# Kernel optimization log

Measured on AMD Instinct MI355X. Metric: run time of the kernel, lower is better.

The kernel has to match this reference:

```python
import jax, jax.numpy as jnp
import numpy as np

HID, LAT, B, T, E, NB, V = 256, 128, 32, 32, 2048, 10, 6
M = T * E + 1  # message buffer rows; row 0 = zero padding


def _linear_params(key, fan_in, fan_out):
    k1, k2 = jax.random.split(key)
    w = jax.random.normal(k1, (fan_out, fan_in), jnp.float32) * 0.05
    b = jax.random.normal(k2, (fan_out,), jnp.float32) * 0.05
    return w, b


def setup_inputs() -> dict:
    key = jax.random.key(0)
    ks = jax.random.split(key, 20)
    inp = {}
    inp["tree_latent_vec"] = jax.random.normal(ks[0], (B, LAT), jnp.float32)
    inp["nei_idx_h"] = jax.random.randint(ks[1], (T, E, NB), 0, M, jnp.int32)
    inp["nei_idx_o"] = jax.random.randint(ks[2], (T, E, NB), 0, M, jnp.int32)
    inp["cur_labels"] = jax.random.randint(ks[3], (T, E), 0, V, jnp.int32)
    inp["contexts"] = jax.random.randint(ks[4], (T, E), 0, B, jnp.int32)
    inp["direction"] = jax.random.randint(ks[5], (T, E), 0, 2, jnp.int32)
    inp["pred_targets_step"] = jax.random.randint(ks[6], (T, E), 0, V, jnp.int32)
    inp["root_labels"] = jax.random.randint(ks[7], (B,), 0, V, jnp.int32)
    inp["root_nei_idx"] = jax.random.randint(ks[8], (B, NB), 0, M, jnp.int32)
    inp["Wz_w"], inp["Wz_b"] = _linear_params(ks[9], HID + V, HID)
    inp["Wr_w"], inp["Wr_b"] = _linear_params(ks[10], V, HID)
    inp["Ur_w"], inp["Ur_b"] = _linear_params(ks[11], HID, HID)
    inp["Wh_w"], inp["Wh_b"] = _linear_params(ks[12], HID + V, HID)
    inp["W_w"], inp["W_b"] = _linear_params(ks[13], HID + LAT, HID)
    inp["Wo_w"], inp["Wo_b"] = _linear_params(ks[14], HID, V)
    inp["U_w"], inp["U_b"] = _linear_params(ks[15], HID + LAT, HID)
    inp["Uo_w"], inp["Uo_b"] = _linear_params(ks[16], HID, 1)
    inp["Ui_w"], inp["Ui_b"] = _linear_params(ks[17], HID + V, HID)
    return inp


def reference(tree_latent_vec, Wz_w, Wz_b, Wr_w, Wr_b, Ur_w, Ur_b, Wh_w, Wh_b,
              W_w, W_b, Wo_w, Wo_b, U_w, U_b, Uo_w, Uo_b, Ui_w, Ui_b,
              nei_idx_h, nei_idx_o, cur_labels, contexts, direction,
              pred_targets_step, root_labels, root_nei_idx):
    cur_x_all = jax.nn.one_hot(cur_labels, V, dtype=jnp.float32)  # [T,E,V]

    def gru(x, h_nei):  # JTNN tree-GRU: x [E,V], h_nei [E,NB,HID]
        sum_h = h_nei.sum(axis=1)
        z = jax.nn.sigmoid(jnp.concatenate([x, sum_h], -1) @ Wz_w.T + Wz_b)
        r = jax.nn.sigmoid((x @ Wr_w.T + Wr_b)[:, None, :]
                           + h_nei @ Ur_w.T + Ur_b)
        gated = (r * h_nei).sum(axis=1)
        pre_h = jnp.tanh(jnp.concatenate([x, gated], -1) @ Wh_w.T + Wh_b)
        return (1.0 - z) * sum_h + z * pre_h

    def step(H, xs):
        t, nih, nio, x = xs
        h_nei = H[nih]                   # [E,NB,HID] gather
        new_h = gru(x, h_nei)            # [E,HID]
        cur_o = H[nio].sum(axis=1)       # [E,HID]
        write_idx = 1 + t * E + jnp.arange(E, dtype=jnp.int32)
        H = H.at[write_idx].set(new_h)   # scatter new messages
        return H, (new_h, cur_o)

    H0 = jnp.zeros((M, HID), jnp.float32)
    ts = jnp.arange(T, dtype=jnp.int32)
    H_final, (new_h_all, cur_o_all) = jax.lax.scan(
        step, H0, (ts, nei_idx_h, nei_idx_o, cur_x_all))

    # ---- word (pred) head ----
    pred_hid = jnp.concatenate(
        [jnp.zeros((B, HID), jnp.float32), new_h_all.reshape(-1, HID)], 0)
    pred_ctx = jnp.concatenate(
        [jnp.arange(B, dtype=jnp.int32), contexts.reshape(-1)], 0)
    pred_tgt = jnp.concatenate([root_labels, pred_targets_step.reshape(-1)], 0)
    pred_mask = jnp.concatenate(
        [jnp.ones((B,), jnp.float32),
         (direction.reshape(-1) == 1).astype(jnp.float32)], 0)
    inp = jnp.concatenate([pred_hid, tree_latent_vec[pred_ctx]], -1)
    pred_scores = jax.nn.relu(inp @ W_w.T + W_b) @ Wo_w.T + Wo_b  # [N,V]
    logp = jax.nn.log_softmax(pred_scores, axis=-1)
    ce = -jnp.take_along_axis(logp, pred_tgt[:, None], axis=1)[:, 0]
    pred_loss = jnp.sum(ce * pred_mask) / B
    preds = jnp.argmax(pred_scores, axis=1)
    pred_acc = jnp.sum((preds == pred_tgt).astype(jnp.float32) * pred_mask) \
        / jnp.sum(pred_mask)

    # ---- stop head ----
    root_x = jax.nn.one_hot(root_labels, V, dtype=jnp.float32)
    root_o = H_final[root_nei_idx].sum(axis=1)                    # [B,HID]
    stop_hid = jnp.concatenate(
        [jnp.concatenate([cur_x_all, cur_o_all], -1).reshape(-1, V + HID),
         jnp.concatenate([root_x, root_o], -1)], 0)
    stop_ctx = jnp.concatenate(
        [contexts.reshape(-1), jnp.arange(B, dtype=jnp.int32)], 0)
    stop_tgt = jnp.concatenate(
        [direction.reshape(-1).astype(jnp.float32),
         jnp.zeros((B,), jnp.float32)], 0)
    h1 = jax.nn.relu(stop_hid @ Ui_w.T + Ui_b)
    inp2 = jnp.concatenate([h1, tree_latent_vec[stop_ctx]], -1)
    s = (jax.nn.relu(inp2 @ U_w.T + U_b) @ Uo_w.T + Uo_b)[:, 0]
    # BCEWithLogits, reduction='sum'
    stop_loss = jnp.sum(jnp.maximum(s, 0.0) - s * stop_tgt
                        + jnp.log1p(jnp.exp(-jnp.abs(s)))) / B
    stops = (s >= 0).astype(jnp.float32)
    stop_acc = jnp.mean((stops == stop_tgt).astype(jnp.float32))

    return jnp.stack([pred_loss, stop_loss,
                      jax.lax.stop_gradient(pred_acc),
                      jax.lax.stop_gradient(stop_acc)])
```

## Files before the change

kernel.cpp:

```cpp
#include <hip/hip_runtime.h>
#include <math.h>

#define HID 256
#define LAT 128
#define BB  32
#define TT  32
#define EE  2048
#define NBR 10
#define VV  6
#define TE  (TT*EE)
#define NROWS (TE + BB)
#define MROWS (TE + 1)

typedef __attribute__((ext_vector_type(8))) short bfrag;
typedef __attribute__((ext_vector_type(4))) float ffrag;

__device__ __forceinline__ float sigmoidf_(float x) { return 1.0f / (1.0f + expf(-x)); }

__device__ __forceinline__ float bf2f(unsigned short u) {
    union { unsigned int i; float f; } x; x.i = ((unsigned int)u) << 16; return x.f;
}
__device__ __forceinline__ unsigned short f2bf(float f) {
    union { float f; unsigned int i; } x; x.f = f;
    unsigned int r = x.i + 0x7FFFu + ((x.i >> 16) & 1u);
    return (unsigned short)(r >> 16);
}

__global__ __launch_bounds__(256) void prep_all(
    const float* __restrict__ Wz, const float* __restrict__ Wh,
    const float* __restrict__ Ur, const float* __restrict__ Ui,
    const float* __restrict__ Ww, const float* __restrict__ Uw,
    unsigned short* __restrict__ dWz, unsigned short* __restrict__ dWh,
    unsigned short* __restrict__ dUr, unsigned short* __restrict__ dUi,
    unsigned short* __restrict__ dWw, unsigned short* __restrict__ dUw)
{
    const int n = blockIdx.x, k = threadIdx.x;
    const float* s; unsigned short* d; int ldw, koff;
    switch (blockIdx.y) {
        case 0:  s = Wz; d = dWz; ldw = 262; koff = VV; break;
        case 1:  s = Wh; d = dWh; ldw = 262; koff = VV; break;
        case 2:  s = Ur; d = dUr; ldw = 256; koff = 0;  break;
        case 3:  s = Ui; d = dUi; ldw = 262; koff = VV; break;
        case 4:  s = Ww; d = dWw; ldw = 384; koff = 0;  break;
        default: s = Uw; d = dUw; ldw = 384; koff = 0;  break;
    }
    d[n * 256 + k] = f2bf(s[(size_t)n * ldw + koff + k]);
}

__global__ __launch_bounds__(256) void prep_cols(
    const float* __restrict__ Wz_w, const float* __restrict__ Wz_b,
    const float* __restrict__ Wh_w, const float* __restrict__ Wh_b,
    const float* __restrict__ Wr_w, const float* __restrict__ Wr_b,
    const float* __restrict__ Ur_b,
    const float* __restrict__ Ui_w, const float* __restrict__ Ui_b,
    float* __restrict__ zcol, float* __restrict__ hcol,
    float* __restrict__ rcol, float* __restrict__ icol)
{
    const int v = blockIdx.x, h = threadIdx.x;
    zcol[v * 256 + h] = Wz_w[h * 262 + v] + Wz_b[h];
    hcol[v * 256 + h] = Wh_w[h * 262 + v] + Wh_b[h];
    rcol[v * 256 + h] = Wr_w[h * VV + v] + Wr_b[h] + Ur_b[h];
    icol[v * 256 + h] = Ui_w[h * 262 + v] + Ui_b[h];
}

__global__ __launch_bounds__(256) void lat_gemm2(
    const float* __restrict__ lat,
    const float* __restrict__ W0, const float* __restrict__ W1,
    float* __restrict__ out0, float* __restrict__ out1)
{
    const int b = blockIdx.x, h = threadIdx.x;
    const float* W = blockIdx.y ? W1 : W0;
    float* out     = blockIdx.y ? out1 : out0;
    float acc = 0.f;
    #pragma unroll 4
    for (int k = 0; k < LAT; ++k)
        acc += lat[b * LAT + k] * W[h * 384 + 256 + k];
    out[b * 256 + h] = acc;
}

#define SFP 268
#define SHP 280

__global__ __launch_bounds__(512) void step_fused(
    const unsigned short* __restrict__ Hb,
    const unsigned short* __restrict__ Ub,
    const int* __restrict__ nih, const int* __restrict__ nio,
    const int* __restrict__ labels,
    const float* __restrict__ rcol, const float* __restrict__ zcol,
    const float* __restrict__ hcol,
    const unsigned short* __restrict__ Wzb,
    const unsigned short* __restrict__ Whb,
    const unsigned short* __restrict__ Urb,
    unsigned short* __restrict__ HbW, unsigned short* __restrict__ UbW,
    unsigned short* __restrict__ curOb,
    int rowg_base)
{
    __shared__ float          s_sum[16][SFP];
    __shared__ unsigned short s_gat[16][SHP];
    __shared__ unsigned short s_nh [16][SHP];
    __shared__ int s_idxh[16][NBR];
    __shared__ int s_idxo[16][NBR];
    __shared__ int s_lbl[16];

    const int tid = threadIdx.x;
    const int e0  = blockIdx.x * 16;

    if (tid < 160) {
        s_idxh[tid / NBR][tid % NBR] = nih[e0 * NBR + tid];
        s_idxo[tid / NBR][tid % NBR] = nio[e0 * NBR + tid];
    }
    if (tid >= 160 && tid < 176) s_lbl[tid - 160] = labels[e0 + tid - 160];
    __syncthreads();

    const int w = tid >> 6;
    const int l = tid & 63;

    {
        const int el = w * 2 + (l >> 5);
        const int h0 = (l & 31) * 8;
        float s[8], g[8], o[8], rc[8];
        #pragma unroll
        for (int j = 0; j < 8; ++j) { s[j] = 0.f; g[j] = 0.f; o[j] = 0.f; }
        const int lb = s_lbl[el];
        #pragma unroll
        for (int j = 0; j < 8; ++j) rc[j] = rcol[lb * 256 + h0 + j];

        #pragma unroll
        for (int nb = 0; nb < NBR; ++nb) {
            const int ih = s_idxh[el][nb];
            if ((unsigned)(ih - rowg_base) >= (unsigned)EE) {
                uint4 hv = *reinterpret_cast<const uint4*>(Hb + (size_t)ih * 256 + h0);
                uint4 uv = *reinterpret_cast<const uint4*>(Ub + (size_t)ih * 256 + h0);
                const unsigned short* hp = reinterpret_cast<const unsigned short*>(&hv);
                const unsigned short* up = reinterpret_cast<const unsigned short*>(&uv);
                #pragma unroll
                for (int j = 0; j < 8; ++j) {
                    const float hf = bf2f(hp[j]);
                    s[j] += hf;
                    g[j] += hf * sigmoidf_(rc[j] + bf2f(up[j]));
                }
            }
            const int io = s_idxo[el][nb];
            if ((unsigned)(io - rowg_base) >= (unsigned)EE) {
                uint4 ov = *reinterpret_cast<const uint4*>(Hb + (size_t)io * 256 + h0);
                const unsigned short* op = reinterpret_cast<const unsigned short*>(&ov);
                #pragma unroll
                for (int j = 0; j < 8; ++j) o[j] += bf2f(op[j]);
            }
        }
        *reinterpret_cast<float4*>(&s_sum[el][h0])     = make_float4(s[0], s[1], s[2], s[3]);
        *reinterpret_cast<float4*>(&s_sum[el][h0 + 4]) = make_float4(s[4], s[5], s[6], s[7]);
        union { unsigned short u[8]; uint4 v; } gu, ou;
        #pragma unroll
        for (int j = 0; j < 8; ++j) { gu.u[j] = f2bf(g[j]); ou.u[j] = f2bf(o[j]); }
        *reinterpret_cast<uint4*>(&s_gat[el][h0]) = gu.v;
        *reinterpret_cast<uint4*>(curOb + (size_t)(e0 + el) * 256 + h0) = ou.v;
    }
    __syncthreads();

    const int ar  = l & 15;
    const int kg  = (l >> 4) * 8;
    const int nb0 = w * 32;

    ffrag zacc[2], pacc[2];
    #pragma unroll
    for (int nt = 0; nt < 2; ++nt) {
        zacc[nt] = (ffrag){0.f, 0.f, 0.f, 0.f};
        pacc[nt] = (ffrag){0.f, 0.f, 0.f, 0.f};
    }
    #pragma unroll
    for (int ks = 0; ks < 8; ++ks) {
        const int k0 = ks * 32 + kg;
        bfrag az;
        const float* ap = &s_sum[ar][k0];
        #pragma unroll
        for (int j = 0; j < 8; ++j) az[j] = (short)f2bf(ap[j]);
        bfrag ah = *reinterpret_cast<const bfrag*>(&s_gat[ar][k0]);
        #pragma unroll
        for (int nt = 0; nt < 2; ++nt) {
            const int n = nb0 + nt * 16 + ar;
            bfrag bz = *reinterpret_cast<const bfrag*>(Wzb + (size_t)n * 256 + k0);
            bfrag bh = *reinterpret_cast<const bfrag*>(Whb + (size_t)n * 256 + k0);
            zacc[nt] = __builtin_amdgcn_mfma_f32_16x16x32_bf16(az, bz, zacc[nt], 0, 0, 0);
            pacc[nt] = __builtin_amdgcn_mfma_f32_16x16x32_bf16(ah, bh, pacc[nt], 0, 0, 0);
        }
    }

    #pragma unroll
    for (int nt = 0; nt < 2; ++nt) {
        const int n = nb0 + nt * 16 + (l & 15);
        #pragma unroll
        for (int r = 0; r < 4; ++r) {
            const int m  = (l >> 4) * 4 + r;
            const int lb = s_lbl[m];
            const float z  = sigmoidf_(zacc[nt][r] + zcol[lb * 256 + n]);
            const float ph = tanhf(pacc[nt][r] + hcol[lb * 256 + n]);
            const float nh = (1.f - z) * s_sum[m][n] + z * ph;
            s_nh[m][n] = f2bf(nh);
        }
    }
    __syncthreads();

    {
        const int row = tid >> 5, c8 = (tid & 31) * 8;
        uint4 v = *reinterpret_cast<const uint4*>(&s_nh[row][c8]);
        *reinterpret_cast<uint4*>(HbW + (size_t)(rowg_base + e0 + row) * 256 + c8) = v;
    }

    ffrag uacc[2];
    #pragma unroll
    for (int nt = 0; nt < 2; ++nt) uacc[nt] = (ffrag){0.f, 0.f, 0.f, 0.f};
    #pragma unroll
    for (int ks = 0; ks < 8; ++ks) {
        const int k0 = ks * 32 + kg;
        bfrag a = *reinterpret_cast<const bfrag*>(&s_nh[ar][k0]);
        #pragma unroll
        for (int nt = 0; nt < 2; ++nt) {
            const int n = nb0 + nt * 16 + ar;
            bfrag b = *reinterpret_cast<const bfrag*>(Urb + (size_t)n * 256 + k0);
            uacc[nt] = __builtin_amdgcn_mfma_f32_16x16x32_bf16(a, b, uacc[nt], 0, 0, 0);
        }
    }
    #pragma unroll
    for (int nt = 0; nt < 2; ++nt) {
        const int n = nb0 + nt * 16 + (l & 15);
        #pragma unroll
        for (int r = 0; r < 4; ++r) {
            const int m = (l >> 4) * 4 + r;
            s_gat[m][n] = f2bf(uacc[nt][r]);
        }
    }
    __syncthreads();
    {
        const int row = tid >> 5, c8 = (tid & 31) * 8;
        uint4 v = *reinterpret_cast<const uint4*>(&s_gat[row][c8]);
        *reinterpret_cast<uint4*>(UbW + (size_t)(rowg_base + e0 + row) * 256 + c8) = v;
    }
}

template<int EPI>
__global__ __launch_bounds__(256) void hgemm(
    const unsigned short* __restrict__ A, int M,
    const unsigned short* __restrict__ Wb,
    const int* __restrict__ lab1, const int* __restrict__ lab2,
    const float* __restrict__ icol,
    unsigned short* __restrict__ C)
{
    __shared__ unsigned short sbuf[64 * 264];
    __shared__ int s_lb[64];

    const int tid = threadIdx.x;
    const int m0  = blockIdx.x * 64;

    if (EPI == 1 && tid < 64) {
        const int r = m0 + tid;
        int lb = 0;
        if (r < M) lb = (r < TE) ? lab1[r] : lab2[r - TE];
        s_lb[tid] = lb;
    }

    const int w  = tid >> 6;
    const int l  = tid & 63;
    const int ar = l & 15;
    const int kg = (l >> 4) * 8;
    const int lrow = tid >> 2;
    const int lcol = (tid & 3) * 8;

    ffrag acc[4][4];
    #pragma unroll
    for (int mt = 0; mt < 4; ++mt)
        #pragma unroll
        for (int nt = 0; nt < 4; ++nt)
            acc[mt][nt] = (ffrag){0.f, 0.f, 0.f, 0.f};

    for (int kc = 0; kc < 8; ++kc) {
        const int k0 = kc * 32;
        uint4 av = make_uint4(0u, 0u, 0u, 0u);
        if (m0 + lrow < M)
            av = *reinterpret_cast<const uint4*>(A + (size_t)(m0 + lrow) * 256 + k0 + lcol);
        if (kc) __syncthreads();
        *reinterpret_cast<uint4*>(&sbuf[lrow * 40 + lcol]) = av;
        __syncthreads();
        bfrag a[4];
        #pragma unroll
        for (int mt = 0; mt < 4; ++mt)
            a[mt] = *reinterpret_cast<const bfrag*>(&sbuf[(mt * 16 + ar) * 40 + kg]);
        #pragma unroll
        for (int nt = 0; nt < 4; ++nt) {
            const int n = w * 64 + nt * 16 + ar;
            bfrag b = *reinterpret_cast<const bfrag*>(Wb + (size_t)n * 256 + k0 + kg);
            #pragma unroll
            for (int mt = 0; mt < 4; ++mt)
                acc[mt][nt] = __builtin_amdgcn_mfma_f32_16x16x32_bf16(a[mt], b, acc[mt][nt], 0, 0, 0);
        }
    }
    __syncthreads();

    #pragma unroll
    for (int mt = 0; mt < 4; ++mt) {
        #pragma unroll
        for (int nt = 0; nt < 4; ++nt) {
            const int n = w * 64 + nt * 16 + (l & 15);
            #pragma unroll
            for (int r = 0; r < 4; ++r) {
                const int m = mt * 16 + (l >> 4) * 4 + r;
                float v = acc[mt][nt][r];
                if (EPI == 1) v = fmaxf(v + icol[s_lb[m] * 256 + n], 0.f);
                sbuf[m * 264 + n] = f2bf(v);
            }
        }
    }
    __syncthreads();
    {
        const int row = tid >> 2;
        const int cb  = (tid & 3) * 64;
        if (m0 + row < M) {
            #pragma unroll
            for (int q = 0; q < 8; ++q) {
                const int col = cb + q * 8;
                uint4 v = *reinterpret_cast<const uint4*>(&sbuf[row * 264 + col]);
                *reinterpret_cast<uint4*>(C + (size_t)(m0 + row) * 256 + col) = v;
            }
        }
    }
}

__global__ __launch_bounds__(256) void root_o_kernel(
    const unsigned short* __restrict__ Hb, const int* __restrict__ rni,
    unsigned short* __restrict__ dst)
{
    const int b = blockIdx.x, h = threadIdx.x;
    float o = 0.f;
    #pragma unroll
    for (int nb = 0; nb < NBR; ++nb)
        o += bf2f(Hb[(size_t)rni[b * NBR + nb] * 256 + h]);
    dst[(size_t)b * 256 + h] = f2bf(o);
}

__global__ __launch_bounds__(256) void pred_head(
    const unsigned short* __restrict__ pre, const float* __restrict__ latW,
    const float* __restrict__ W_b,
    const float* __restrict__ Wo_w, const float* __restrict__ Wo_b,
    const int* __restrict__ contexts, const int* __restrict__ direction,
    const int* __restrict__ ptgt, const int* __restrict__ root_labels,
    float* __restrict__ part)
{
    const int r = blockIdx.x;
    const int h = threadIdx.x;
    int tgt;
    float mask, v;
    if (r < TE) {
        const int c = contexts[r];
        tgt = ptgt[r];
        mask = (direction[r] == 1) ? 1.f : 0.f;
        v = bf2f(pre[(size_t)r * 256 + h]) + latW[c * 256 + h] + W_b[h];
    } else {
        const int i = r - TE;
        tgt = root_labels[i];
        mask = 1.f;
        v = latW[i * 256 + h] + W_b[h];
    }
    v = fmaxf(v, 0.f);

    __shared__ float red[VV][4];
    const int lane = h & 63, wv = h >> 6;
    #pragma unroll
    for (int c = 0; c < VV; ++c) {
        float x = v * Wo_w[c * 256 + h];
        #pragma unroll
        for (int off = 32; off; off >>= 1) x += __shfl_down(x, off);
        if (lane == 0) red[c][wv] = x;
    }
    __syncthreads();
    if (h == 0) {
        float sc[VV];
        #pragma unroll
        for (int c = 0; c < VV; ++c)
            sc[c] = red[c][0] + red[c][1] + red[c][2] + red[c][3] + Wo_b[c];
        float mx = sc[0];
        int am = 0;
        #pragma unroll
        for (int c = 1; c < VV; ++c)
            if (sc[c] > mx) { mx = sc[c]; am = c; }
        float se = 0.f;
        #pragma unroll
        for (int c = 0; c < VV; ++c) se += expf(sc[c] - mx);
        const float lse = mx + logf(se);
        const float ce = lse - sc[tgt];
        part[(size_t)r * 3 + 0] = ce * mask;
        part[(size_t)r * 3 + 1] = mask;
        part[(size_t)r * 3 + 2] = (am == tgt) ? mask : 0.f;
    }
}

__global__ __launch_bounds__(256) void stop_head(
    const unsigned short* __restrict__ pre2, const float* __restrict__ latW2,
    const float* __restrict__ U_b,
    const float* __restrict__ Uo_w, const float* __restrict__ Uo_b,
    const int* __restrict__ contexts, const int* __restrict__ direction,
    float* __restrict__ part2)
{
    const int r = blockIdx.x;
    const int h = threadIdx.x;
    const int c = (r < TE) ? contexts[r] : (r - TE);
    const float tgt = (r < TE) ? (float)direction[r] : 0.f;
    float v = fmaxf(bf2f(pre2[(size_t)r * 256 + h]) + latW2[c * 256 + h] + U_b[h], 0.f);
    float x = v * Uo_w[h];
    #pragma unroll
    for (int off = 32; off; off >>= 1) x += __shfl_down(x, off);
    __shared__ float red[4];
    const int lane = h & 63, wv = h >> 6;
    if (lane == 0) red[wv] = x;
    __syncthreads();
    if (h == 0) {
        const float s = red[0] + red[1] + red[2] + red[3] + Uo_b[0];
        const float loss = fmaxf(s, 0.f) - s * tgt + log1pf(expf(-fabsf(s)));
        const float stop = (s >= 0.f) ? 1.f : 0.f;
        part2[(size_t)r * 2 + 0] = loss;
        part2[(size_t)r * 2 + 1] = (stop == tgt) ? 1.f : 0.f;
    }
}

__global__ __launch_bounds__(256) void reduce_parts(
    const float* __restrict__ p1, const float* __restrict__ p2,
    float* __restrict__ accum)
{
    float a[5] = {0.f, 0.f, 0.f, 0.f, 0.f};
    const int stride = gridDim.x * blockDim.x;
    for (int r = blockIdx.x * blockDim.x + threadIdx.x; r < NROWS; r += stride) {
        a[0] += p1[(size_t)r * 3 + 0];
        a[1] += p1[(size_t)r * 3 + 1];
        a[2] += p1[(size_t)r * 3 + 2];
        a[3] += p2[(size_t)r * 2 + 0];
        a[4] += p2[(size_t)r * 2 + 1];
    }
    __shared__ float red[5][4];
    const int lane = threadIdx.x & 63, wv = threadIdx.x >> 6;
    #pragma unroll
    for (int i = 0; i < 5; ++i) {
        float x = a[i];
        #pragma unroll
        for (int off = 32; off; off >>= 1) x += __shfl_down(x, off);
        if (lane == 0) red[i][wv] = x;
    }
    __syncthreads();
    if (threadIdx.x < 5) {
        const float s = red[threadIdx.x][0] + red[threadIdx.x][1] +
                        red[threadIdx.x][2] + red[threadIdx.x][3];
        atomicAdd(&accum[threadIdx.x], s);
    }
}

__global__ void finalize(const float* __restrict__ accum, float* __restrict__ out)
{
    if (threadIdx.x == 0) {
        out[0] = accum[0] / (float)BB;
        out[1] = accum[3] / (float)BB;
        out[2] = accum[2] / accum[1];
        out[3] = accum[4] / (float)NROWS;
    }
}

extern "C" void kernel_launch(void* const* d_in, const int* in_sizes, int n_in,
                              void* d_out, int out_size, void* d_ws, size_t ws_size,
                              hipStream_t stream)
{
    const float* lat  = (const float*)d_in[0];
    const int*   nih  = (const int*)d_in[1];
    const int*   nio  = (const int*)d_in[2];
    const int*   lbl  = (const int*)d_in[3];
    const int*   ctx  = (const int*)d_in[4];
    const int*   dir  = (const int*)d_in[5];
    const int*   ptg  = (const int*)d_in[6];
    const int*   rlb  = (const int*)d_in[7];
    const int*   rni  = (const int*)d_in[8];
    const float* Wz_w = (const float*)d_in[9],  *Wz_b = (const float*)d_in[10];
    const float* Wr_w = (const float*)d_in[11], *Wr_b = (const float*)d_in[12];
    const float* Ur_w = (const float*)d_in[13], *Ur_b = (const float*)d_in[14];
    const float* Wh_w = (const float*)d_in[15], *Wh_b = (const float*)d_in[16];
    const float* W_w  = (const float*)d_in[17], *W_b  = (const float*)d_in[18];
    const float* Wo_w = (const float*)d_in[19], *Wo_b = (const float*)d_in[20];
    const float* U_w  = (const float*)d_in[21], *U_b  = (const float*)d_in[22];
    const float* Uo_w = (const float*)d_in[23], *Uo_b = (const float*)d_in[24];
    const float* Ui_w = (const float*)d_in[25], *Ui_b = (const float*)d_in[26];

    char* p = (char*)d_ws;
    auto alloc = [&](size_t bytes) -> void* {
        void* r = (void*)p; p += (bytes + 255) & ~(size_t)255; return r;
    };
    const size_t RB2 = (size_t)NROWS * 256 * sizeof(unsigned short);
    unsigned short* Hb    = (unsigned short*)alloc(RB2);
    unsigned short* Ub    = (unsigned short*)alloc(RB2);
    unsigned short* curOb = (unsigned short*)alloc(RB2);
    unsigned short* h1b   = (unsigned short*)alloc(RB2);
    unsigned short* pre2b = (unsigned short*)alloc(RB2);
    unsigned short* Wzb = (unsigned short*)alloc(65536 * 2);
    unsigned short* Whb = (unsigned short*)alloc(65536 * 2);
    unsigned short* Urb = (unsigned short*)alloc(65536 * 2);
    unsigned short* Uib = (unsigned short*)alloc(65536 * 2);
    unsigned short* Wwb = (unsigned short*)alloc(65536 * 2);
    unsigned short* Uwb = (unsigned short*)alloc(65536 * 2);
    float* zcol  = (float*)alloc(VV * 256 * 4);
    float* hcol  = (float*)alloc(VV * 256 * 4);
    float* rcol  = (float*)alloc(VV * 256 * 4);
    float* icol  = (float*)alloc(VV * 256 * 4);
    float* latW  = (float*)alloc(BB * 256 * 4);
    float* latW2 = (float*)alloc(BB * 256 * 4);
    float* part1 = (float*)alloc((size_t)NROWS * 3 * 4);
    float* part2 = (float*)alloc((size_t)NROWS * 2 * 4);
    float* accum = (float*)alloc(32);

    hipMemsetAsync(Hb, 0, RB2, stream);
    hipMemsetAsync(Ub, 0, RB2, stream);
    hipMemsetAsync(accum, 0, 32, stream);

    prep_all<<<dim3(256, 6), 256, 0, stream>>>(Wz_w, Wh_w, Ur_w, Ui_w, W_w, U_w,
                                               Wzb, Whb, Urb, Uib, Wwb, Uwb);
    prep_cols<<<VV, 256, 0, stream>>>(Wz_w, Wz_b, Wh_w, Wh_b, Wr_w, Wr_b, Ur_b,
                                      Ui_w, Ui_b, zcol, hcol, rcol, icol);
    lat_gemm2<<<dim3(BB, 2), 256, 0, stream>>>(lat, W_w, U_w, latW, latW2);

    for (int t = 0; t < TT; ++t) {
        step_fused<<<EE / 16, 512, 0, stream>>>(
            Hb, Ub, nih + (size_t)t * EE * NBR, nio + (size_t)t * EE * NBR,
            lbl + t * EE, rcol, zcol, hcol, Wzb, Whb, Urb,
            Hb, Ub, curOb + (size_t)t * EE * 256, 1 + t * EE);
    }

    root_o_kernel<<<BB, 256, 0, stream>>>(Hb, rni, curOb + (size_t)TE * 256);

    hgemm<1><<<(NROWS + 63) / 64, 256, 0, stream>>>(curOb, NROWS, Uib, lbl, rlb, icol, h1b);
    hgemm<0><<<(NROWS + 63) / 64, 256, 0, stream>>>(h1b, NROWS, Uwb, nullptr, nullptr, nullptr, pre2b);
    stop_head<<<NROWS, 256, 0, stream>>>(pre2b, latW2, U_b, Uo_w, Uo_b, ctx, dir, part2);

    hgemm<0><<<TE / 64, 256, 0, stream>>>(Hb + 256, TE, Wwb, nullptr, nullptr, nullptr, h1b);
    pred_head<<<NROWS, 256, 0, stream>>>(h1b, latW, W_b, Wo_w, Wo_b,
                                         ctx, dir, ptg, rlb, part1);

    reduce_parts<<<256, 256, 0, stream>>>(part1, part2, accum);
    finalize<<<1, 64, 0, stream>>>(accum, (float*)d_out);
}
```

Measured before the change: 1.433 ms.

## Halve step_fused tile to 8 edges and batch head kernels 64 rows per block

The recurrent step kernel now handles 8 edges per 256-thread block instead of 16 per 512 threads, which doubles the grid to 256 blocks per step. Each wave computes 64 output columns, and the unused upper half of the 16-row MFMA tile is zero-padded. The pred and stop heads change from one 256-thread block per row with shuffle reductions to 64-thread blocks that stage 64 rows in shared memory, with one thread computing each row's dot products. This is meant to improve CU occupancy in the latency-bound step loop and to cut per-row block overhead in the heads. The cost is MFMA work wasted on the padding rows and serial per-thread dot products in the heads.

Result: faster. 1.316 ms (-8.2%).

```diff
diff --git a/kernel.cpp b/kernel.cpp
--- a/kernel.cpp
+++ b/kernel.cpp
@@ -81,7 +81,7 @@
 #define SFP 268
 #define SHP 280
 
-__global__ __launch_bounds__(512) void step_fused(
+__global__ __launch_bounds__(256) void step_fused(
     const unsigned short* __restrict__ Hb,
     const unsigned short* __restrict__ Ub,
     const int* __restrict__ nih, const int* __restrict__ nio,
@@ -98,26 +98,38 @@
     __shared__ float          s_sum[16][SFP];
     __shared__ unsigned short s_gat[16][SHP];
     __shared__ unsigned short s_nh [16][SHP];
-    __shared__ int s_idxh[16][NBR];
-    __shared__ int s_idxo[16][NBR];
+    __shared__ int s_idxh[8][NBR];
+    __shared__ int s_idxo[8][NBR];
     __shared__ int s_lbl[16];
 
     const int tid = threadIdx.x;
-    const int e0  = blockIdx.x * 16;
-
-    if (tid < 160) {
+    const int e0  = blockIdx.x * 8;
+
+    if (tid < 80) {
         s_idxh[tid / NBR][tid % NBR] = nih[e0 * NBR + tid];
-        s_idxo[tid / NBR][tid % NBR] = nio[e0 * NBR + tid];
-    }
-    if (tid >= 160 && tid < 176) s_lbl[tid - 160] = labels[e0 + tid - 160];
+    } else if (tid < 160) {
+        const int t = tid - 80;
+        s_idxo[t / NBR][t % NBR] = nio[e0 * NBR + t];
+    } else if (tid < 176) {
+        const int t = tid - 160;
+        s_lbl[t] = (t < 8) ? labels[e0 + t] : 0;
+    }
+    {
+        const int zr = 8 + (tid >> 5), zd = (tid & 31) * 8;
+        *reinterpret_cast<float4*>(&s_sum[zr][zd])     = make_float4(0.f, 0.f, 0.f, 0.f);
+        *reinterpret_cast<float4*>(&s_sum[zr][zd + 4]) = make_float4(0.f, 0.f, 0.f, 0.f);
+        const uint4 z4 = make_uint4(0u, 0u, 0u, 0u);
+        *reinterpret_cast<uint4*>(&s_gat[zr][zd]) = z4;
+        *reinterpret_cast<uint4*>(&s_nh [zr][zd]) = z4;
+    }
     __syncthreads();
 
     const int w = tid >> 6;
     const int l = tid & 63;
 
     {
-        const int el = w * 2 + (l >> 5);
-        const int h0 = (l & 31) * 8;
+        const int el = tid >> 5;
+        const int h0 = (tid & 31) * 8;
         float s[8], g[8], o[8], rc[8];
         #pragma unroll
         for (int j = 0; j < 8; ++j) { s[j] = 0.f; g[j] = 0.f; o[j] = 0.f; }
@@ -160,11 +172,11 @@
 
     const int ar  = l & 15;
     const int kg  = (l >> 4) * 8;
-    const int nb0 = w * 32;
-
-    ffrag zacc[2], pacc[2];
-    #pragma unroll
-    for (int nt = 0; nt < 2; ++nt) {
+    const int nb0 = w * 64;
+
+    ffrag zacc[4], pacc[4];
+    #pragma unroll
+    for (int nt = 0; nt < 4; ++nt) {
         zacc[nt] = (ffrag){0.f, 0.f, 0.f, 0.f};
         pacc[nt] = (ffrag){0.f, 0.f, 0.f, 0.f};
     }
@@ -177,7 +189,7 @@
         for (int j = 0; j < 8; ++j) az[j] = (short)f2bf(ap[j]);
         bfrag ah = *reinterpret_cast<const bfrag*>(&s_gat[ar][k0]);
         #pragma unroll
-        for (int nt = 0; nt < 2; ++nt) {
+        for (int nt = 0; nt < 4; ++nt) {
             const int n = nb0 + nt * 16 + ar;
             bfrag bz = *reinterpret_cast<const bfrag*>(Wzb + (size_t)n * 256 + k0);
             bfrag bh = *reinterpret_cast<const bfrag*>(Whb + (size_t)n * 256 + k0);
@@ -187,16 +199,18 @@
     }
 
     #pragma unroll
-    for (int nt = 0; nt < 2; ++nt) {
+    for (int nt = 0; nt < 4; ++nt) {
         const int n = nb0 + nt * 16 + (l & 15);
         #pragma unroll
         for (int r = 0; r < 4; ++r) {
-            const int m  = (l >> 4) * 4 + r;
-            const int lb = s_lbl[m];
-            const float z  = sigmoidf_(zacc[nt][r] + zcol[lb * 256 + n]);
-            const float ph = tanhf(pacc[nt][r] + hcol[lb * 256 + n]);
-            const float nh = (1.f - z) * s_sum[m][n] + z * ph;
-            s_nh[m][n] = f2bf(nh);
+            const int m = (l >> 4) * 4 + r;
+            if (m < 8) {
+                const int lb = s_lbl[m];
+                const float z  = sigmoidf_(zacc[nt][r] + zcol[lb * 256 + n]);
+                const float ph = tanhf(pacc[nt][r] + hcol[lb * 256 + n]);
+                const float nh = (1.f - z) * s_sum[m][n] + z * ph;
+                s_nh[m][n] = f2bf(nh);
+            }
         }
     }
     __syncthreads();
@@ -207,27 +221,27 @@
         *reinterpret_cast<uint4*>(HbW + (size_t)(rowg_base + e0 + row) * 256 + c8) = v;
     }
 
-    ffrag uacc[2];
-    #pragma unroll
-    for (int nt = 0; nt < 2; ++nt) uacc[nt] = (ffrag){0.f, 0.f, 0.f, 0.f};
+    ffrag uacc[4];
+    #pragma unroll
+    for (int nt = 0; nt < 4; ++nt) uacc[nt] = (ffrag){0.f, 0.f, 0.f, 0.f};
     #pragma unroll
     for (int ks = 0; ks < 8; ++ks) {
         const int k0 = ks * 32 + kg;
         bfrag a = *reinterpret_cast<const bfrag*>(&s_nh[ar][k0]);
         #pragma unroll
-        for (int nt = 0; nt < 2; ++nt) {
+        for (int nt = 0; nt < 4; ++nt) {
             const int n = nb0 + nt * 16 + ar;
             bfrag b = *reinterpret_cast<const bfrag*>(Urb + (size_t)n * 256 + k0);
             uacc[nt] = __builtin_amdgcn_mfma_f32_16x16x32_bf16(a, b, uacc[nt], 0, 0, 0);
         }
     }
     #pragma unroll
-    for (int nt = 0; nt < 2; ++nt) {
+    for (int nt = 0; nt < 4; ++nt) {
         const int n = nb0 + nt * 16 + (l & 15);
         #pragma unroll
         for (int r = 0; r < 4; ++r) {
             const int m = (l >> 4) * 4 + r;
-            s_gat[m][n] = f2bf(uacc[nt][r]);
+            if (m < 8) s_gat[m][n] = f2bf(uacc[nt][r]);
         }
     }
     __syncthreads();
@@ -337,7 +351,7 @@
     dst[(size_t)b * 256 + h] = f2bf(o);
 }
 
-__global__ __launch_bounds__(256) void pred_head(
+__global__ __launch_bounds__(64) void pred_head(
     const unsigned short* __restrict__ pre, const float* __restrict__ latW,
     const float* __restrict__ W_b,
     const float* __restrict__ Wo_w, const float* __restrict__ Wo_b,
@@ -345,80 +359,137 @@
     const int* __restrict__ ptgt, const int* __restrict__ root_labels,
     float* __restrict__ part)
 {
-    const int r = blockIdx.x;
-    const int h = threadIdx.x;
-    int tgt;
-    float mask, v;
-    if (r < TE) {
-        const int c = contexts[r];
-        tgt = ptgt[r];
-        mask = (direction[r] == 1) ? 1.f : 0.f;
-        v = bf2f(pre[(size_t)r * 256 + h]) + latW[c * 256 + h] + W_b[h];
+    __shared__ unsigned short sv[64][264];
+    const int l  = threadIdx.x;
+    const int r0 = blockIdx.x * 64;
+
+    for (int it = 0; it < 32; ++it) {
+        const int rr  = it * 2 + (l >> 5);
+        const int row = r0 + rr;
+        const int d0  = (l & 31) * 8;
+        float v[8];
+        if (row < NROWS) {
+            const int c = (row < TE) ? contexts[row] : (row - TE);
+            uint4 pv = make_uint4(0u, 0u, 0u, 0u);
+            if (row < TE)
+                pv = *reinterpret_cast<const uint4*>(pre + (size_t)row * 256 + d0);
+            const unsigned short* pp = reinterpret_cast<const unsigned short*>(&pv);
+            const float4 la = *reinterpret_cast<const float4*>(latW + c * 256 + d0);
+            const float4 lb = *reinterpret_cast<const float4*>(latW + c * 256 + d0 + 4);
+            const float4 ba = *reinterpret_cast<const float4*>(W_b + d0);
+            const float4 bb = *reinterpret_cast<const float4*>(W_b + d0 + 4);
+            const float lv[8] = {la.x, la.y, la.z, la.w, lb.x, lb.y, lb.z, lb.w};
+            const float bv[8] = {ba.x, ba.y, ba.z, ba.w, bb.x, bb.y, bb.z, bb.w};
+            #pragma unroll
+            for (int j = 0; j < 8; ++j) {
+                float x = lv[j] + bv[j];
+                if (row < TE) x += bf2f(pp[j]);
+                v[j] = fmaxf(x, 0.f);
+            }
+        } else {
+            #pragma unroll
+            for (int j = 0; j < 8; ++j) v[j] = 0.f;
+        }
+        union { unsigned short u[8]; uint4 q; } uu;
+        #pragma unroll
+        for (int j = 0; j < 8; ++j) uu.u[j] = f2bf(v[j]);
+        *reinterpret_cast<uint4*>(&sv[rr][d0]) = uu.q;
+    }
+    __syncthreads();
+
+    const int row = r0 + l;
+    if (row >= NROWS) return;
+    float sc[VV];
+    #pragma unroll
+    for (int c = 0; c < VV; ++c) sc[c] = Wo_b[c];
+    for (int it = 0; it < 32; ++it) {
+        const int d0 = it * 8;
+        bfrag vv = *reinterpret_cast<const bfrag*>(&sv[l][d0]);
+        #pragma unroll
+        for (int j = 0; j < 8; ++j) {
+            const float x = bf2f((unsigned short)vv[j]);
+            #pragma unroll
+            for (int c = 0; c < VV; ++c)
+                sc[c] += x * Wo_w[c * 256 + d0 + j];
+        }
+    }
+    int tgt; float mask;
+    if (row < TE) {
+        tgt  = ptgt[row];
+        mask = (direction[row] == 1) ? 1.f : 0.f;
     } else {
-        const int i = r - TE;
-        tgt = root_labels[i];
+        tgt  = root_labels[row - TE];
         mask = 1.f;
-        v = latW[i * 256 + h] + W_b[h];
-    }
-    v = fmaxf(v, 0.f);
-
-    __shared__ float red[VV][4];
-    const int lane = h & 63, wv = h >> 6;
-    #pragma unroll
-    for (int c = 0; c < VV; ++c) {
-        float x = v * Wo_w[c * 256 + h];
-        #pragma unroll
-        for (int off = 32; off; off >>= 1) x += __shfl_down(x, off);
-        if (lane == 0) red[c][wv] = x;
-    }
-    __syncthreads();
-    if (h == 0) {
-        float sc[VV];
-        #pragma unroll
-        for (int c = 0; c < VV; ++c)
-            sc[c] = red[c][0] + red[c][1] + red[c][2] + red[c][3] + Wo_b[c];
-        float mx = sc[0];
-        int am = 0;
-        #pragma unroll
-        for (int c = 1; c < VV; ++c)
-            if (sc[c] > mx) { mx = sc[c]; am = c; }
-        float se = 0.f;
-        #pragma unroll
-        for (int c = 0; c < VV; ++c) se += expf(sc[c] - mx);
-        const float lse = mx + logf(se);
-        const float ce = lse - sc[tgt];
-        part[(size_t)r * 3 + 0] = ce * mask;
-        part[(size_t)r * 3 + 1] = mask;
-        part[(size_t)r * 3 + 2] = (am == tgt) ? mask : 0.f;
-    }
-}
-
-__global__ __launch_bounds__(256) void stop_head(
+    }
+    float mx = sc[0]; int am = 0;
+    #pragma unroll
+    for (int c = 1; c < VV; ++c)
+        if (sc[c] > mx) { mx = sc[c]; am = c; }
+    float se = 0.f;
+    #pragma unroll
+    for (int c = 0; c < VV; ++c) se += expf(sc[c] - mx);
+    const float lse = mx + logf(se);
+    const float ce = lse - sc[tgt];
+    part[(size_t)row * 3 + 0] = ce * mask;
+    part[(size_t)row * 3 + 1] = mask;
+    part[(size_t)row * 3 + 2] = (am == tgt) ? mask : 0.f;
+}
+
+__global__ __launch_bounds__(64) void stop_head(
     const unsigned short* __restrict__ pre2, const float* __restrict__ latW2,
     const float* __restrict__ U_b,
     const float* __restrict__ Uo_w, const float* __restrict__ Uo_b,
     const int* __restrict__ contexts, const int* __restrict__ direction,
     float* __restrict__ part2)
 {
-    const int r = blockIdx.x;
-    const int h = threadIdx.x;
-    const int c = (r < TE) ? contexts[r] : (r - TE);
-    const float tgt = (r < TE) ? (float)direction[r] : 0.f;
-    float v = fmaxf(bf2f(pre2[(size_t)r * 256 + h]) + latW2[c * 256 + h] + U_b[h], 0.f);
-    float x = v * Uo_w[h];
-    #pragma unroll
-    for (int off = 32; off; off >>= 1) x += __shfl_down(x, off);
-    __shared__ float red[4];
-    const int lane = h & 63, wv = h >> 6;
-    if (lane == 0) red[wv] = x;
-    __syncthreads();
-    if (h == 0) {
-        const float s = red[0] + red[1] + red[2] + red[3] + Uo_b[0];
-        const float loss = fmaxf(s, 0.f) - s * tgt + log1pf(expf(-fabsf(s)));
-        const float stop = (s >= 0.f) ? 1.f : 0.f;
-        part2[(size_t)r * 2 + 0] = loss;
-        part2[(size_t)r * 2 + 1] = (stop == tgt) ? 1.f : 0.f;
-    }
+    __shared__ unsigned short sv[64][264];
+    const int l  = threadIdx.x;
+    const int r0 = blockIdx.x * 64;
+
+    for (int it = 0; it < 32; ++it) {
+        const int rr  = it * 2 + (l >> 5);
+        const int row = r0 + rr;
+        const int d0  = (l & 31) * 8;
+        float v[8];
+        if (row < NROWS) {
+            const int c = (row < TE) ? contexts[row] : (row - TE);
+            uint4 pv = *reinterpret_cast<const uint4*>(pre2 + (size_t)row * 256 + d0);
+            const unsigned short* pp = reinterpret_cast<const unsigned short*>(&pv);
+            const float4 la = *reinterpret_cast<const float4*>(latW2 + c * 256 + d0);
+            const float4 lb = *reinterpret_cast<const float4*>(latW2 + c * 256 + d0 + 4);
+            const float4 ba = *reinterpret_cast<const float4*>(U_b + d0);
+            const float4 bb = *reinterpret_cast<const float4*>(U_b + d0 + 4);
+            const float lv[8] = {la.x, la.y, la.z, la.w, lb.x, lb.y, lb.z, lb.w};
+            const float bv[8] = {ba.x, ba.y, ba.z, ba.w, bb.x, bb.y, bb.z, bb.w};
+            #pragma unroll
+            for (int j = 0; j < 8; ++j)
+                v[j] = fmaxf(bf2f(pp[j]) + lv[j] + bv[j], 0.f);
+        } else {
+            #pragma unroll
+            for (int j = 0; j < 8; ++j) v[j] = 0.f;
+        }
+        union { unsigned short u[8]; uint4 q; } uu;
+        #pragma unroll
+        for (int j = 0; j < 8; ++j) uu.u[j] = f2bf(v[j]);
+        *reinterpret_cast<uint4*>(&sv[rr][d0]) = uu.q;
+    }
+    __syncthreads();
+
+    const int row = r0 + l;
+    if (row >= NROWS) return;
+    float s = Uo_b[0];
+    for (int it = 0; it < 32; ++it) {
+        const int d0 = it * 8;
+        bfrag vv = *reinterpret_cast<const bfrag*>(&sv[l][d0]);
+        #pragma unroll
+        for (int j = 0; j < 8; ++j)
+            s += bf2f((unsigned short)vv[j]) * Uo_w[d0 + j];
+    }
+    const float tgt = (row < TE) ? (float)direction[row] : 0.f;
+    const float loss = fmaxf(s, 0.f) - s * tgt + log1pf(expf(-fabsf(s)));
+    const float stop = (s >= 0.f) ? 1.f : 0.f;
+    part2[(size_t)row * 2 + 0] = loss;
+    part2[(size_t)row * 2 + 1] = (stop == tgt) ? 1.f : 0.f;
 }
 
 __global__ __launch_bounds__(256) void reduce_parts(
@@ -521,7 +592,7 @@
     lat_gemm2<<<dim3(BB, 2), 256, 0, stream>>>(lat, W_w, U_w, latW, latW2);
 
     for (int t = 0; t < TT; ++t) {
-        step_fused<<<EE / 16, 512, 0, stream>>>(
+        step_fused<<<EE / 8, 256, 0, stream>>>(
             Hb, Ub, nih + (size_t)t * EE * NBR, nio + (size_t)t * EE * NBR,
             lbl + t * EE, rcol, zcol, hcol, Wzb, Whb, Urb,
             Hb, Ub, curOb + (size_t)t * EE * 256, 1 + t * EE);
@@ -531,11 +602,11 @@
 
     hgemm<1><<<(NROWS + 63) / 64, 256, 0, stream>>>(curOb, NROWS, Uib, lbl, rlb, icol, h1b);
     hgemm<0><<<(NROWS + 63) / 64, 256, 0, stream>>>(h1b, NROWS, Uwb, nullptr, nullptr, nullptr, pre2b);
-    stop_head<<<NROWS, 256, 0, stream>>>(pre2b, latW2, U_b, Uo_w, Uo_b, ctx, dir, part2);
+    stop_head<<<(NROWS + 63) / 64, 64, 0, stream>>>(pre2b, latW2, U_b, Uo_w, Uo_b, ctx, dir, part2);
 
     hgemm<0><<<TE / 64, 256, 0, stream>>>(Hb + 256, TE, Wwb, nullptr, nullptr, nullptr, h1b);
-    pred_head<<<NROWS, 256, 0, stream>>>(h1b, latW, W_b, Wo_w, Wo_b,
-                                         ctx, dir, ptg, rlb, part1);
+    pred_head<<<(NROWS + 63) / 64, 64, 0, stream>>>(h1b, latW, W_b, Wo_w, Wo_b,
+                                                    ctx, dir, ptg, rlb, part1);
 
     reduce_parts<<<256, 256, 0, stream>>>(part1, part2, accum);
     finalize<<<1, 64, 0, stream>>>(accum, (float*)d_out);
```
